# Performance work log

Measured on AMD Instinct MI355X. Metric: run time of the kernel, lower is better.

The kernel has to match this reference:

```python
import jax, jax.numpy as jnp
import numpy as np

N = 100000   # nodes
E = 1600000  # edges
IN_CH = 128
EDGE_DIM = 16
HEADS = 4
OUT_CH = 16
NEG_SLOPE = 0.2


def setup_inputs() -> dict:
    key = jax.random.key(0)
    ks = jax.random.split(key, 12)
    HC = HEADS * OUT_CH
    inp = {
        "x": jax.random.normal(ks[0], (N, IN_CH), dtype=jnp.float32),
        "edge_index": jax.random.randint(ks[1], (2, E), 0, N, dtype=jnp.int32),
        "edge_attr": jax.random.normal(ks[2], (E, EDGE_DIM), dtype=jnp.float32),
        # linear layer params (W stored as [in, out] so y = x @ W + b)
        "W_src": jax.random.normal(ks[3], (IN_CH, HC), dtype=jnp.float32) / np.sqrt(IN_CH),
        "b_src": jnp.zeros((HC,), dtype=jnp.float32),
        "W_dst": jax.random.normal(ks[4], (IN_CH, HC), dtype=jnp.float32) / np.sqrt(IN_CH),
        "b_dst": jnp.zeros((HC,), dtype=jnp.float32),
        "W_edge": jax.random.normal(ks[5], (EDGE_DIM, HC), dtype=jnp.float32) / np.sqrt(EDGE_DIM),
        "b_edge": jnp.zeros((HC,), dtype=jnp.float32),
        # attention vectors [1, heads, out_channels]
        "att_src": jax.random.normal(ks[6], (1, HEADS, OUT_CH), dtype=jnp.float32) * 0.1,
        "att_dst": jax.random.normal(ks[7], (1, HEADS, OUT_CH), dtype=jnp.float32) * 0.1,
        "att_edge": jax.random.normal(ks[8], (1, HEADS, OUT_CH), dtype=jnp.float32) * 0.1,
    }
    return inp


def _segment_softmax(alpha, seg, num_segments):
    # alpha: [E, H]; softmax over edges sharing the same dst node (seg).
    m = jax.ops.segment_max(alpha, seg, num_segments=num_segments)
    m = jnp.where(jnp.isfinite(m), m, 0.0)  # empty segments -> -inf; neutralize
    a = jnp.exp(alpha - m[seg])
    s = jax.ops.segment_sum(a, seg, num_segments=num_segments)
    return a / (s[seg] + 1e-16)


def reference(x, edge_index, edge_attr, W_src, b_src, W_dst, b_dst,
              W_edge, b_edge, att_src, att_dst, att_edge):
    n = x.shape[0]
    src_idx, dst_idx = edge_index[0], edge_index[1]

    src = (x @ W_src + b_src).reshape(n, HEADS, OUT_CH)        # [N,H,C]
    dst = (x @ W_dst + b_dst).reshape(n, HEADS, OUT_CH)        # [N,H,C]
    edge_feat = (edge_attr @ W_edge + b_edge).reshape(-1, HEADS, OUT_CH)  # [E,H,C]

    alpha_src = jnp.sum(src * att_src, axis=-1)[src_idx]       # [E,H]
    alpha_dst = jnp.sum(dst * att_dst, axis=-1)[dst_idx]       # [E,H]
    alpha_edge = jnp.sum(edge_feat * att_edge, axis=-1)        # [E,H]

    alpha = alpha_src + alpha_dst + alpha_edge
    alpha = jnp.where(alpha >= 0, alpha, NEG_SLOPE * alpha)    # leaky_relu(0.2)
    alpha = _segment_softmax(alpha, dst_idx, n)                # [E,H]
    # dropout is identity in eval mode

    msg = src[src_idx] * alpha[..., None]                      # [E,H,C]
    out = jax.ops.segment_sum(msg, dst_idx, num_segments=n)    # [N,H,C]
    return out.reshape(n, HEADS * OUT_CH)
```

## Files before the change

kernel.cpp:

```cpp
#include <hip/hip_runtime.h>


#define N_NODES 100000
#define N_EDGES 1600000
#define SCAN_B 1024
#define SCAN_NBLK ((N_NODES + SCAN_B - 1) / SCAN_B)

static __device__ __forceinline__ unsigned int f2bf(float f) {
    unsigned int u = __float_as_uint(f);
    return (u + 0x7fffu + ((u >> 16) & 1u)) >> 16;
}
static __device__ __forceinline__ float bf2f(unsigned int bits16) {
    return __uint_as_float(bits16 << 16);
}

__global__ __launch_bounds__(256) void k_node_proj(
    const float* __restrict__ x, const float* __restrict__ Wsrc,
    const float* __restrict__ bsrc, const float* __restrict__ Wdst,
    const float* __restrict__ bdst, const float* __restrict__ att_src,
    const float* __restrict__ att_dst, unsigned short* __restrict__ spbf,
    float* __restrict__ alpha_sn, float* __restrict__ alpha_dn)
{
    __shared__ float xs[32 * 128];
    const int tid = threadIdx.x;
    const int nbase = blockIdx.x * 32;

    const float4* xsrc = (const float4*)(x + (size_t)nbase * 128);
    float4* xd = (float4*)xs;
#pragma unroll
    for (int i = 0; i < 4; ++i)
        xd[tid + i * 256] = xsrc[tid + i * 256];
    __syncthreads();

    const int col = tid & 63;
    const int g = tid >> 6;

    float accS[8], accD[8];
#pragma unroll
    for (int i = 0; i < 8; ++i) { accS[i] = 0.f; accD[i] = 0.f; }

    for (int k4 = 0; k4 < 128; k4 += 4) {
        float4 xv[8];
#pragma unroll
        for (int i = 0; i < 8; ++i)
            xv[i] = *(const float4*)&xs[(g * 8 + i) * 128 + k4];
#pragma unroll
        for (int kk = 0; kk < 4; ++kk) {
            float wsv = Wsrc[(k4 + kk) * 64 + col];
            float wdv = Wdst[(k4 + kk) * 64 + col];
#pragma unroll
            for (int i = 0; i < 8; ++i) {
                float xvk = ((const float*)&xv[i])[kk];
                accS[i] = fmaf(xvk, wsv, accS[i]);
                accD[i] = fmaf(xvk, wdv, accD[i]);
            }
        }
    }

    const float bs = bsrc[col], bd = bdst[col];
    const float as_ = att_src[col], ad_ = att_dst[col];
    const int h = col >> 4;
#pragma unroll
    for (int i = 0; i < 8; ++i) {
        const int n = nbase + g * 8 + i;
        float vS = accS[i] + bs;
        float vD = accD[i] + bd;
        spbf[(size_t)n * 64 + col] = (unsigned short)f2bf(vS);
        float t1 = vS * as_;
        float t2 = vD * ad_;
#pragma unroll
        for (int off = 8; off >= 1; off >>= 1) {
            t1 += __shfl_xor(t1, off, 16);
            t2 += __shfl_xor(t2, off, 16);
        }
        if ((col & 15) == 0) {
            alpha_sn[n * 4 + h] = t1;
            alpha_dn[n * 4 + h] = t2;
        }
    }
}

__global__ void k_prep(const float* __restrict__ We, const float* __restrict__ be,
                       const float* __restrict__ att_e, float* __restrict__ V)
{
    const int t = threadIdx.x;
    const int k = t >> 2, h = t & 3;
    float acc = 0.f;
    for (int c = 0; c < 16; ++c)
        acc += We[k * 64 + h * 16 + c] * att_e[h * 16 + c];
    V[k * 4 + h] = acc;
    if (t < 4) {
        float b = 0.f;
        for (int c = 0; c < 16; ++c)
            b += be[t * 16 + c] * att_e[t * 16 + c];
        V[64 + t] = b;
    }
}

__global__ __launch_bounds__(256) void k_hist(const int* __restrict__ ei,
                                               int* __restrict__ cnt)
{
    const int e = blockIdx.x * 256 + threadIdx.x;
    if (e >= N_EDGES) return;
    atomicAdd(&cnt[ei[N_EDGES + e]], 1);
}

__global__ __launch_bounds__(256) void k_scan_part(const int* __restrict__ cnt,
                                                    int* __restrict__ partial)
{
    __shared__ int red[4];
    const int t = threadIdx.x;
    const int base = blockIdx.x * SCAN_B + t * 4;
    int s = 0;
#pragma unroll
    for (int i = 0; i < 4; ++i) {
        const int idx = base + i;
        if (idx < N_NODES) s += cnt[idx];
    }
#pragma unroll
    for (int off = 32; off >= 1; off >>= 1)
        s += __shfl_xor(s, off, 64);
    if ((t & 63) == 0) red[t >> 6] = s;
    __syncthreads();
    if (t == 0)
        partial[blockIdx.x] = red[0] + red[1] + red[2] + red[3];
}

__global__ __launch_bounds__(128) void k_scan_top(int* __restrict__ partial)
{
    __shared__ int sums[128];
    const int t = threadIdx.x;
    sums[t] = (t < SCAN_NBLK) ? partial[t] : 0;
    __syncthreads();
#pragma unroll
    for (int off = 1; off < 128; off <<= 1) {
        int v = (t >= off) ? sums[t - off] : 0;
        __syncthreads();
        sums[t] += v;
        __syncthreads();
    }
    if (t < SCAN_NBLK) partial[t] = (t == 0) ? 0 : sums[t - 1];
}

__global__ __launch_bounds__(256) void k_scan_down(
    const int* __restrict__ cnt, const int* __restrict__ partial,
    int* __restrict__ row_start, int* __restrict__ cursor)
{
    __shared__ int tsum[256];
    const int t = threadIdx.x;
    const int base = blockIdx.x * SCAN_B + t * 4;
    int c[4];
#pragma unroll
    for (int i = 0; i < 4; ++i) {
        const int idx = base + i;
        c[i] = (idx < N_NODES) ? cnt[idx] : 0;
    }
    const int tot = c[0] + c[1] + c[2] + c[3];
    tsum[t] = tot;
    __syncthreads();
#pragma unroll
    for (int off = 1; off < 256; off <<= 1) {
        int v = (t >= off) ? tsum[t - off] : 0;
        __syncthreads();
        tsum[t] += v;
        __syncthreads();
    }
    int run = partial[blockIdx.x] + ((t == 0) ? 0 : tsum[t - 1]);
#pragma unroll
    for (int i = 0; i < 4; ++i) {
        const int idx = base + i;
        if (idx < N_NODES) {
            row_start[idx] = run;
            cursor[idx] = run;
        }
        run += c[i];
    }
    if (blockIdx.x == 0 && t == 0)
        row_start[N_NODES] = N_EDGES;
}

__global__ __launch_bounds__(256) void k_fill(
    const int* __restrict__ ei, const float* __restrict__ ea,
    const float* __restrict__ V, const float* __restrict__ alpha_sn,
    const float* __restrict__ alpha_dn, int* __restrict__ cursor,
    int4* __restrict__ rec)
{
    __shared__ float Vs[68];
    if (threadIdx.x < 68) Vs[threadIdx.x] = V[threadIdx.x];
    __syncthreads();

    const int e = blockIdx.x * 256 + threadIdx.x;
    if (e >= N_EDGES) return;
    const int src = ei[e];
    const int dst = ei[N_EDGES + e];

    const float4* ea4 = (const float4*)(ea + (size_t)e * 16);
    float ek[16];
    {
        float4 c0 = ea4[0], c1 = ea4[1], c2 = ea4[2], c3 = ea4[3];
        ek[0]=c0.x; ek[1]=c0.y; ek[2]=c0.z; ek[3]=c0.w;
        ek[4]=c1.x; ek[5]=c1.y; ek[6]=c1.z; ek[7]=c1.w;
        ek[8]=c2.x; ek[9]=c2.y; ek[10]=c2.z; ek[11]=c2.w;
        ek[12]=c3.x; ek[13]=c3.y; ek[14]=c3.z; ek[15]=c3.w;
    }
    float a[4] = {Vs[64], Vs[65], Vs[66], Vs[67]};
#pragma unroll
    for (int k = 0; k < 16; ++k) {
#pragma unroll
        for (int h = 0; h < 4; ++h)
            a[h] = fmaf(ek[k], Vs[k * 4 + h], a[h]);
    }

    const float4 asn = *(const float4*)(alpha_sn + (size_t)src * 4);
    const float4 adn = *(const float4*)(alpha_dn + (size_t)dst * 4);
    float a0 = a[0] + asn.x + adn.x;
    float a1 = a[1] + asn.y + adn.y;
    float a2 = a[2] + asn.z + adn.z;
    float a3 = a[3] + asn.w + adn.w;
    a0 = (a0 >= 0.f) ? a0 : 0.2f * a0;
    a1 = (a1 >= 0.f) ? a1 : 0.2f * a1;
    a2 = (a2 >= 0.f) ? a2 : 0.2f * a2;
    a3 = (a3 >= 0.f) ? a3 : 0.2f * a3;

    const unsigned int w01 = f2bf(__expf(a0)) | (f2bf(__expf(a1)) << 16);
    const unsigned int w23 = f2bf(__expf(a2)) | (f2bf(__expf(a3)) << 16);

    const int slot = atomicAdd(&cursor[dst], 1);
    rec[slot] = make_int4(src, (int)w01, (int)w23, 0);
}

__global__ __launch_bounds__(256) void k_gather(
    const int* __restrict__ row_start, const int4* __restrict__ rec,
    const unsigned short* __restrict__ spbf, float* __restrict__ out)
{
    const int lane = threadIdx.x & 63;
    const int node = (blockIdx.x * 256 + threadIdx.x) >> 6;
    const int h = lane >> 4;
    const int base = row_start[node];
    const int end = row_start[node + 1];

    float acc = 0.f, denom = 0.f;
    int j = base;
    for (; j + 4 <= end; j += 4) {
        const int4 r0 = rec[j], r1 = rec[j + 1], r2 = rec[j + 2], r3 = rec[j + 3];
        const float v0 = bf2f(spbf[((size_t)r0.x << 6) + lane]);
        const float v1 = bf2f(spbf[((size_t)r1.x << 6) + lane]);
        const float v2 = bf2f(spbf[((size_t)r2.x << 6) + lane]);
        const float v3 = bf2f(spbf[((size_t)r3.x << 6) + lane]);
#define WEXT(r) bf2f(((h & 1) ? ((unsigned int)((h < 2) ? r.y : r.z) >> 16) \
                              : ((unsigned int)((h < 2) ? r.y : r.z) & 0xffffu)))
        const float w0 = WEXT(r0), w1 = WEXT(r1), w2 = WEXT(r2), w3 = WEXT(r3);
        denom += (w0 + w1) + (w2 + w3);
        acc = fmaf(w0, v0, acc);
        acc = fmaf(w1, v1, acc);
        acc = fmaf(w2, v2, acc);
        acc = fmaf(w3, v3, acc);
    }
    for (; j < end; ++j) {
        const int4 r0 = rec[j];
        const float v0 = bf2f(spbf[((size_t)r0.x << 6) + lane]);
        const float w0 = WEXT(r0);
        denom += w0;
        acc = fmaf(w0, v0, acc);
    }
#undef WEXT
    out[(size_t)node * 64 + lane] = acc / (denom + 1e-16f);
}

extern "C" void kernel_launch(void* const* d_in, const int* in_sizes, int n_in,
                              void* d_out, int out_size, void* d_ws, size_t ws_size,
                              hipStream_t stream) {
    const float* x     = (const float*)d_in[0];
    const int*   ei    = (const int*)d_in[1];
    const float* ea    = (const float*)d_in[2];
    const float* Wsrc  = (const float*)d_in[3];
    const float* bsrc  = (const float*)d_in[4];
    const float* Wdst  = (const float*)d_in[5];
    const float* bdst  = (const float*)d_in[6];
    const float* We    = (const float*)d_in[7];
    const float* be    = (const float*)d_in[8];
    const float* att_s = (const float*)d_in[9];
    const float* att_d = (const float*)d_in[10];
    const float* att_e = (const float*)d_in[11];
    float* out = (float*)d_out;

    int4*  rec       = (int4*)d_ws;
    unsigned short* spbf = (unsigned short*)(rec + N_EDGES);
    float* alpha_sn  = (float*)(spbf + (size_t)N_NODES * 64);
    float* alpha_dn  = alpha_sn + (size_t)N_NODES * 4;
    int*   cnt       = (int*)(alpha_dn + (size_t)N_NODES * 4);
    int*   row_start = cnt + N_NODES;
    int*   cursor    = row_start + N_NODES + 4;
    int*   partial   = cursor + N_NODES;
    float* V         = (float*)(partial + 128);

    hipMemsetAsync(cnt, 0, (size_t)N_NODES * sizeof(int), stream);

    k_node_proj<<<N_NODES / 32, 256, 0, stream>>>(x, Wsrc, bsrc, Wdst, bdst,
                                                  att_s, att_d, spbf,
                                                  alpha_sn, alpha_dn);
    k_prep<<<1, 64, 0, stream>>>(We, be, att_e, V);
    k_hist<<<N_EDGES / 256, 256, 0, stream>>>(ei, cnt);
    k_scan_part<<<SCAN_NBLK, 256, 0, stream>>>(cnt, partial);
    k_scan_top<<<1, 128, 0, stream>>>(partial);
    k_scan_down<<<SCAN_NBLK, 256, 0, stream>>>(cnt, partial, row_start, cursor);
    k_fill<<<N_EDGES / 256, 256, 0, stream>>>(ei, ea, V, alpha_sn, alpha_dn,
                                              cursor, rec);
    k_gather<<<(N_NODES + 3) / 4, 256, 0, stream>>>(row_start, rec, spbf, out);
}
```

Before: 484.9 us.

## Record per-edge rank in histogram pass and add nontemporal loads/stores

The histogram kernel now keeps the return value of its atomic increment as a per-edge rank. The fill kernel computes each slot as row_start[dst] + rank, which removes the second round of atomics on a cursor array and the cursor initialisation in the scan. Streaming loads and stores across several kernels are switched to nontemporal builtins to reduce cache pollution. In exchange the code writes and reads an extra 6.4 MB rank array, and nontemporal hints on the rec records read by the gather could hurt reuse.

```diff
diff --git a/kernel.cpp b/kernel.cpp
--- a/kernel.cpp
+++ b/kernel.cpp
@@ -5,6 +5,9 @@
 #define N_EDGES 1600000
 #define SCAN_B 1024
 #define SCAN_NBLK ((N_NODES + SCAN_B - 1) / SCAN_B)
+
+typedef int   v4i __attribute__((ext_vector_type(4)));
+typedef float v4f __attribute__((ext_vector_type(4)));
 
 static __device__ __forceinline__ unsigned int f2bf(float f) {
     unsigned int u = __float_as_uint(f);
@@ -25,11 +28,11 @@
     const int tid = threadIdx.x;
     const int nbase = blockIdx.x * 32;
 
-    const float4* xsrc = (const float4*)(x + (size_t)nbase * 128);
-    float4* xd = (float4*)xs;
+    const v4f* xsrc = (const v4f*)(x + (size_t)nbase * 128);
+    v4f* xd = (v4f*)xs;
 #pragma unroll
     for (int i = 0; i < 4; ++i)
-        xd[tid + i * 256] = xsrc[tid + i * 256];
+        xd[tid + i * 256] = __builtin_nontemporal_load(xsrc + tid + i * 256);
     __syncthreads();
 
     const int col = tid & 63;
@@ -40,17 +43,17 @@
     for (int i = 0; i < 8; ++i) { accS[i] = 0.f; accD[i] = 0.f; }
 
     for (int k4 = 0; k4 < 128; k4 += 4) {
-        float4 xv[8];
+        v4f xv[8];
 #pragma unroll
         for (int i = 0; i < 8; ++i)
-            xv[i] = *(const float4*)&xs[(g * 8 + i) * 128 + k4];
+            xv[i] = *(const v4f*)&xs[(g * 8 + i) * 128 + k4];
 #pragma unroll
         for (int kk = 0; kk < 4; ++kk) {
             float wsv = Wsrc[(k4 + kk) * 64 + col];
             float wdv = Wdst[(k4 + kk) * 64 + col];
 #pragma unroll
             for (int i = 0; i < 8; ++i) {
-                float xvk = ((const float*)&xv[i])[kk];
+                float xvk = xv[i][kk];
                 accS[i] = fmaf(xvk, wsv, accS[i]);
                 accD[i] = fmaf(xvk, wdv, accD[i]);
             }
@@ -98,11 +101,14 @@
 }
 
 __global__ __launch_bounds__(256) void k_hist(const int* __restrict__ ei,
-                                               int* __restrict__ cnt)
+                                               int* __restrict__ cnt,
+                                               int* __restrict__ rank)
 {
     const int e = blockIdx.x * 256 + threadIdx.x;
     if (e >= N_EDGES) return;
-    atomicAdd(&cnt[ei[N_EDGES + e]], 1);
+    const int dst = __builtin_nontemporal_load(&ei[N_EDGES + e]);
+    const int r = atomicAdd(&cnt[dst], 1);
+    __builtin_nontemporal_store(r, &rank[e]);
 }
 
 __global__ __launch_bounds__(256) void k_scan_part(const int* __restrict__ cnt,
@@ -144,7 +150,7 @@
 
 __global__ __launch_bounds__(256) void k_scan_down(
     const int* __restrict__ cnt, const int* __restrict__ partial,
-    int* __restrict__ row_start, int* __restrict__ cursor)
+    int* __restrict__ row_start)
 {
     __shared__ int tsum[256];
     const int t = threadIdx.x;
@@ -169,10 +175,7 @@
 #pragma unroll
     for (int i = 0; i < 4; ++i) {
         const int idx = base + i;
-        if (idx < N_NODES) {
-            row_start[idx] = run;
-            cursor[idx] = run;
-        }
+        if (idx < N_NODES) row_start[idx] = run;
         run += c[i];
     }
     if (blockIdx.x == 0 && t == 0)
@@ -182,8 +185,8 @@
 __global__ __launch_bounds__(256) void k_fill(
     const int* __restrict__ ei, const float* __restrict__ ea,
     const float* __restrict__ V, const float* __restrict__ alpha_sn,
-    const float* __restrict__ alpha_dn, int* __restrict__ cursor,
-    int4* __restrict__ rec)
+    const float* __restrict__ alpha_dn, const int* __restrict__ row_start,
+    const int* __restrict__ rank, v4i* __restrict__ rec)
 {
     __shared__ float Vs[68];
     if (threadIdx.x < 68) Vs[threadIdx.x] = V[threadIdx.x];
@@ -191,17 +194,18 @@
 
     const int e = blockIdx.x * 256 + threadIdx.x;
     if (e >= N_EDGES) return;
-    const int src = ei[e];
-    const int dst = ei[N_EDGES + e];
-
-    const float4* ea4 = (const float4*)(ea + (size_t)e * 16);
+    const int src = __builtin_nontemporal_load(&ei[e]);
+    const int dst = __builtin_nontemporal_load(&ei[N_EDGES + e]);
+
+    const v4f* ea4 = (const v4f*)(ea + (size_t)e * 16);
+    const v4f c0 = __builtin_nontemporal_load(ea4 + 0);
+    const v4f c1 = __builtin_nontemporal_load(ea4 + 1);
+    const v4f c2 = __builtin_nontemporal_load(ea4 + 2);
+    const v4f c3 = __builtin_nontemporal_load(ea4 + 3);
     float ek[16];
-    {
-        float4 c0 = ea4[0], c1 = ea4[1], c2 = ea4[2], c3 = ea4[3];
-        ek[0]=c0.x; ek[1]=c0.y; ek[2]=c0.z; ek[3]=c0.w;
-        ek[4]=c1.x; ek[5]=c1.y; ek[6]=c1.z; ek[7]=c1.w;
-        ek[8]=c2.x; ek[9]=c2.y; ek[10]=c2.z; ek[11]=c2.w;
-        ek[12]=c3.x; ek[13]=c3.y; ek[14]=c3.z; ek[15]=c3.w;
+#pragma unroll
+    for (int i = 0; i < 4; ++i) {
+        ek[i] = c0[i]; ek[4 + i] = c1[i]; ek[8 + i] = c2[i]; ek[12 + i] = c3[i];
     }
     float a[4] = {Vs[64], Vs[65], Vs[66], Vs[67]};
 #pragma unroll
@@ -225,12 +229,14 @@
     const unsigned int w01 = f2bf(__expf(a0)) | (f2bf(__expf(a1)) << 16);
     const unsigned int w23 = f2bf(__expf(a2)) | (f2bf(__expf(a3)) << 16);
 
-    const int slot = atomicAdd(&cursor[dst], 1);
-    rec[slot] = make_int4(src, (int)w01, (int)w23, 0);
+    const int slot = row_start[dst] + __builtin_nontemporal_load(&rank[e]);
+    v4i r;
+    r[0] = src; r[1] = (int)w01; r[2] = (int)w23; r[3] = 0;
+    __builtin_nontemporal_store(r, rec + slot);
 }
 
 __global__ __launch_bounds__(256) void k_gather(
-    const int* __restrict__ row_start, const int4* __restrict__ rec,
+    const int* __restrict__ row_start, const v4i* __restrict__ rec,
     const unsigned short* __restrict__ spbf, float* __restrict__ out)
 {
     const int lane = threadIdx.x & 63;
@@ -242,13 +248,16 @@
     float acc = 0.f, denom = 0.f;
     int j = base;
     for (; j + 4 <= end; j += 4) {
-        const int4 r0 = rec[j], r1 = rec[j + 1], r2 = rec[j + 2], r3 = rec[j + 3];
-        const float v0 = bf2f(spbf[((size_t)r0.x << 6) + lane]);
-        const float v1 = bf2f(spbf[((size_t)r1.x << 6) + lane]);
-        const float v2 = bf2f(spbf[((size_t)r2.x << 6) + lane]);
-        const float v3 = bf2f(spbf[((size_t)r3.x << 6) + lane]);
-#define WEXT(r) bf2f(((h & 1) ? ((unsigned int)((h < 2) ? r.y : r.z) >> 16) \
-                              : ((unsigned int)((h < 2) ? r.y : r.z) & 0xffffu)))
+        const v4i r0 = __builtin_nontemporal_load(rec + j);
+        const v4i r1 = __builtin_nontemporal_load(rec + j + 1);
+        const v4i r2 = __builtin_nontemporal_load(rec + j + 2);
+        const v4i r3 = __builtin_nontemporal_load(rec + j + 3);
+        const float v0 = bf2f(spbf[((size_t)r0[0] << 6) + lane]);
+        const float v1 = bf2f(spbf[((size_t)r1[0] << 6) + lane]);
+        const float v2 = bf2f(spbf[((size_t)r2[0] << 6) + lane]);
+        const float v3 = bf2f(spbf[((size_t)r3[0] << 6) + lane]);
+#define WEXT(r) bf2f(((h & 1) ? ((unsigned int)((h < 2) ? r[1] : r[2]) >> 16) \
+                              : ((unsigned int)((h < 2) ? r[1] : r[2]) & 0xffffu)))
         const float w0 = WEXT(r0), w1 = WEXT(r1), w2 = WEXT(r2), w3 = WEXT(r3);
         denom += (w0 + w1) + (w2 + w3);
         acc = fmaf(w0, v0, acc);
@@ -257,14 +266,15 @@
         acc = fmaf(w3, v3, acc);
     }
     for (; j < end; ++j) {
-        const int4 r0 = rec[j];
-        const float v0 = bf2f(spbf[((size_t)r0.x << 6) + lane]);
+        const v4i r0 = __builtin_nontemporal_load(rec + j);
+        const float v0 = bf2f(spbf[((size_t)r0[0] << 6) + lane]);
         const float w0 = WEXT(r0);
         denom += w0;
         acc = fmaf(w0, v0, acc);
     }
 #undef WEXT
-    out[(size_t)node * 64 + lane] = acc / (denom + 1e-16f);
+    __builtin_nontemporal_store(acc / (denom + 1e-16f),
+                                &out[(size_t)node * 64 + lane]);
 }
 
 extern "C" void kernel_launch(void* const* d_in, const int* in_sizes, int n_in,
@@ -284,14 +294,14 @@
     const float* att_e = (const float*)d_in[11];
     float* out = (float*)d_out;
 
-    int4*  rec       = (int4*)d_ws;
+    v4i*   rec       = (v4i*)d_ws;
     unsigned short* spbf = (unsigned short*)(rec + N_EDGES);
     float* alpha_sn  = (float*)(spbf + (size_t)N_NODES * 64);
     float* alpha_dn  = alpha_sn + (size_t)N_NODES * 4;
-    int*   cnt       = (int*)(alpha_dn + (size_t)N_NODES * 4);
+    int*   rank      = (int*)(alpha_dn + (size_t)N_NODES * 4);
+    int*   cnt       = rank + N_EDGES;
     int*   row_start = cnt + N_NODES;
-    int*   cursor    = row_start + N_NODES + 4;
-    int*   partial   = cursor + N_NODES;
+    int*   partial   = row_start + N_NODES + 4;
     float* V         = (float*)(partial + 128);
 
     hipMemsetAsync(cnt, 0, (size_t)N_NODES * sizeof(int), stream);
@@ -300,11 +310,11 @@
                                                   att_s, att_d, spbf,
                                                   alpha_sn, alpha_dn);
     k_prep<<<1, 64, 0, stream>>>(We, be, att_e, V);
-    k_hist<<<N_EDGES / 256, 256, 0, stream>>>(ei, cnt);
+    k_hist<<<N_EDGES / 256, 256, 0, stream>>>(ei, cnt, rank);
     k_scan_part<<<SCAN_NBLK, 256, 0, stream>>>(cnt, partial);
     k_scan_top<<<1, 128, 0, stream>>>(partial);
-    k_scan_down<<<SCAN_NBLK, 256, 0, stream>>>(cnt, partial, row_start, cursor);
+    k_scan_down<<<SCAN_NBLK, 256, 0, stream>>>(cnt, partial, row_start);
     k_fill<<<N_EDGES / 256, 256, 0, stream>>>(ei, ea, V, alpha_sn, alpha_dn,
-                                              cursor, rec);
+                                              row_start, rank, rec);
     k_gather<<<(N_NODES + 3) / 4, 256, 0, stream>>>(row_start, rec, spbf, out);
 }
```

Result: slower. 504.0 us (+3.9%).
